# Optimization experiments

Measured on AMD Instinct MI355X. Metric: run time of the kernel, lower is better.

## Reference

```python
import jax, jax.numpy as jnp
import numpy as np

N_ITER = 4
NEG = -1e9


def _build_distmask(n):
    # dists='' -> 2 groups: upper triangular (j>i) and lower triangular (j<i); diag excluded
    iu = jnp.triu(jnp.ones((n, n), jnp.float32), 1)
    return jnp.stack([iu, iu.T], axis=0)  # (2, n, n)


def setup_inputs() -> dict:
    key = jax.random.key(0)
    k1, k2, k3 = jax.random.split(key, 3)
    B, N, D, H, G = 16, 256, 128, 8, 64
    x = jax.random.normal(k1, (B, N, D), jnp.float32)
    mask = jnp.ones((B, N), jnp.int32)
    ternary = jax.random.normal(k2, (2, D, D, H), jnp.float32)
    global_ = jax.random.normal(k3, (G, D, H), jnp.float32) / np.sqrt(D).astype(np.float32)
    return {"x": x, "mask": mask, "ternary": ternary, "global_": global_}


def reference(x, mask, ternary, global_):
    # x: (B,N,D) unary scores; mask: (B,N); ternary: (2,D,D,H); global_: (G,D,H)
    B, N, D = x.shape
    dm = _build_distmask(N)                       # (2,N,N)
    m1 = mask != 0                                # (B,N) valid tokens
    m2 = m1[:, :, None] & m1[:, None, :]          # (B,N,N) valid pairs
    pair_bias = jnp.where(m2[:, None, :, :], 0.0, NEG)  # (B,1,N,N); global cols stay unmasked

    Q_Z = x
    for _ in range(N_ITER):
        qz = jax.nn.softmax(Q_Z, axis=-1)         # (B,N,D) q(Z_i)
        # left[k,b,i,c,h] = sum_a qz[b,i,a] * ternary[k,a,c,h]
        left = jnp.einsum('bia,kach->kbich', qz, ternary)
        # H-node scores over local candidates: F[b,h,i,j] = sum_k dm[k,i,j] * sum_c left[k,b,i,c,h] qz[b,j,c]
        Fk = jnp.einsum('kbich,bjc->kbhij', left, qz)
        F = jnp.einsum('kbhij,kij->bhij', Fk, dm) + pair_bias
        # H-node scores over global candidates: G[b,h,i,g] = sum_a qz[b,i,a] global_[g,a,h]
        Gs = jnp.einsum('bia,gah->bhig', qz, global_)
        S = jnp.concatenate([F, Gs], axis=-1)     # (B,H,N,N+G), all-attn: joint softmax
        qh = jax.nn.softmax(S, axis=-1)           # async update: fresh q(H) used for Z update
        qh_loc, qh_glb = qh[..., :N], qh[..., N:]
        qhd = qh_loc[None] * dm[:, None, None]    # (2,B,H,N,N) distance-gated q(H)
        # right[k,b,j,a,h] = sum_c ternary[k,a,c,h] qz[b,j,c]  (message payload toward Z_i)
        right = jnp.einsum('kach,bjc->kbjah', ternary, qz)
        M1 = jnp.einsum('kbhij,kbjah->bia', qhd, right)   # message to dependent Z_i
        M2 = jnp.einsum('kbhij,kbich->bjc', qhd, left)    # message to head Z_j (block_msg=False)
        MG = jnp.einsum('bhig,gah->bia', qh_glb, global_)  # message from global nodes
        Q_Z = x + M1 + M2 + MG                    # regularize_Z=1, stepsize=1, damping=0
    return Q_Z                                    # output_prob=False -> unnormalized scores
```

## Files before the change

kernel.cpp:

```cpp
#include <hip/hip_runtime.h>
#include <hip/hip_bf16.h>

using bf16 = __hip_bfloat16;
typedef __bf16 bf16x8 __attribute__((ext_vector_type(8)));
typedef float f32x4 __attribute__((ext_vector_type(4)));
typedef unsigned short u16x8 __attribute__((ext_vector_type(8)));
typedef unsigned short u16x4 __attribute__((ext_vector_type(4)));

constexpr int B_ = 16, H_ = 8;
constexpr int BN = 4096;
constexpr int SW = 320;
constexpr float FNEG = -1000000000.0f;
constexpr size_t KOFF = (size_t)8 * 16 * 128 * 256;

__device__ __forceinline__ float b2f(bf16 v){ return __bfloat162float(v); }
__device__ __forceinline__ bf16 f2b(float v){ return __float2bfloat16(v); }
__device__ __forceinline__ bf16x8 ldf(const bf16* p){ return *(const bf16x8*)p; }
__device__ __forceinline__ f32x4 mfma16(bf16x8 a, bf16x8 b, f32x4 c){
  return __builtin_amdgcn_mfma_f32_16x16x32_bf16(a, b, c, 0, 0, 0);
}

__global__ __launch_bounds__(256) void k_prep(const float* __restrict__ tern,
                                              const float* __restrict__ glb,
                                              bf16* __restrict__ TL, bf16* __restrict__ TR,
                                              bf16* __restrict__ GB, bf16* __restrict__ GT){
  int t = blockIdx.x*256 + threadIdx.x;
  {
    int kh = t>>14, rest = t&16383;
    int k = kh>>3, h = kh&7;
    int r = rest>>7, cc = rest&127;
    TL[t] = f2b(tern[(((size_t)k*128 + cc)*128 + r)*8 + h]);
    TR[t] = f2b(tern[(((size_t)k*128 + r)*128 + cc)*8 + h]);
  }
  if (t < 65536){
    int h = t>>13, rest = t&8191;
    { int g = rest>>7, a = rest&127;
      GB[t] = f2b(glb[((size_t)g*128 + a)*8 + h]); }
    { int a = rest>>6, g = rest&63;
      GT[t] = f2b(glb[((size_t)g*128 + a)*8 + h]); }
  }
}

__global__ __launch_bounds__(256) void k_softmax_qz(const float* __restrict__ Q,
                                                    bf16* __restrict__ qzb){
  int row = blockIdx.x*4 + (threadIdx.x>>6);
  int lane = threadIdx.x&63;
  const float* q = Q + (size_t)row*128;
  float v0 = q[lane], v1 = q[lane+64];
  float m = fmaxf(v0, v1);
  #pragma unroll
  for (int o=32;o;o>>=1) m = fmaxf(m, __shfl_xor(m, o));
  float e0 = __expf(v0-m), e1 = __expf(v1-m), s = e0+e1;
  #pragma unroll
  for (int o=32;o;o>>=1) s += __shfl_xor(s, o);
  float inv = 1.f/s;
  bf16* o_ = qzb + (size_t)row*128;
  o_[lane] = f2b(e0*inv); o_[lane+64] = f2b(e1*inv);
}

__global__ __launch_bounds__(256) void k_proj(const bf16* __restrict__ qzb,
                                              const bf16* __restrict__ TL,
                                              const bf16* __restrict__ TR,
                                              bf16* __restrict__ left,
                                              bf16* __restrict__ LT2,
                                              bf16* __restrict__ RT2){
  const int z = blockIdx.z; const int kh = z & 15; const bool rightP = z >= 16;
  const int wi = threadIdx.x>>7, wj = (threadIdx.x>>6)&1;
  const int lane = threadIdx.x&63, lr = lane&15, kg = lane>>4;
  const int rb0 = blockIdx.x*64, cb = blockIdx.y*64;
  const int r0 = rb0 + wi*32, c0 = cb + wj*32;
  const bf16* A  = qzb + (size_t)r0*128;
  const bf16* Bb = (rightP ? TR : TL) + ((size_t)kh*128 + c0)*128;
  f32x4 acc[2][2] = {};
  #pragma unroll
  for (int k0=0;k0<128;k0+=32){
    bf16x8 a0 = ldf(A  + (size_t)lr*128      + k0 + kg*8);
    bf16x8 a1 = ldf(A  + (size_t)(lr+16)*128 + k0 + kg*8);
    bf16x8 b0 = ldf(Bb + (size_t)lr*128      + k0 + kg*8);
    bf16x8 b1 = ldf(Bb + (size_t)(lr+16)*128 + k0 + kg*8);
    acc[0][0]=mfma16(a0,b0,acc[0][0]); acc[0][1]=mfma16(a0,b1,acc[0][1]);
    acc[1][0]=mfma16(a1,b0,acc[1][0]); acc[1][1]=mfma16(a1,b1,acc[1][1]);
  }
  __shared__ unsigned short tl[64][68];
  #pragma unroll
  for (int fi=0;fi<2;fi++)
    #pragma unroll
    for (int fj=0;fj<2;fj++){
      u16x4 pk;
      #pragma unroll
      for (int r=0;r<4;r++) pk[r] = __builtin_bit_cast(unsigned short, f2b(acc[fi][fj][r]));
      *(u16x4*)&tl[wj*32 + fj*16 + lr][wi*32 + fi*16 + kg*4] = pk;
    }
  if (!rightP){
    #pragma unroll
    for (int fi=0;fi<2;fi++){
      int rb = r0 + fi*16 + kg*4;
      #pragma unroll
      for (int fj=0;fj<2;fj++){
        int col = c0 + fj*16 + lr;
        #pragma unroll
        for (int r=0;r<4;r++)
          left[((size_t)kh*BN + rb + r)*128 + col] = f2b(acc[fi][fj][r]);
      }
    }
  }
  __syncthreads();
  const int b = rb0 >> 8, jloc = rb0 & 255;
  const int col = threadIdx.x >> 2, seg = threadIdx.x & 3;
  bf16* O = rightP ? RT2 : LT2;
  unsigned short* dst = (unsigned short*)O +
      (((size_t)kh*16 + b)*128 + cb + col)*256 + jloc + seg*16;
  const unsigned short* src = &tl[col][seg*16];
  #pragma unroll
  for (int e=0;e<4;e++) *(u16x4*)(dst + e*4) = *(const u16x4*)(src + e*4);
}

__global__ __launch_bounds__(256) void k_FSM(const bf16* __restrict__ qzb,
                                             const bf16* __restrict__ left,
                                             const bf16* __restrict__ GB,
                                             const int* __restrict__ mask,
                                             bf16* __restrict__ qh,
                                             bf16* __restrict__ qhT2){
  const int bh = blockIdx.y, b = bh>>3, h = bh&7;
  const int ib4 = blockIdx.x;
  const int w = threadIdx.x>>6, lane = threadIdx.x&63;
  const int lr = lane&15, kg = lane>>4;
  const int i0 = ib4*64, iw = i0 + w*16;
  const int fd = iw>>4;
  const bf16* qzB = qzb + (size_t)b*256*128;
  const bf16* L0 = left + ((size_t)h*BN     + b*256 + iw)*128;
  const bf16* L1 = left + ((size_t)(8+h)*BN + b*256 + iw)*128;
  const bf16* GBh = GB + (size_t)h*64*128;
  f32x4 acc[20] = {}; f32x4 accD = {};
  #pragma unroll
  for (int k0=0;k0<128;k0+=32){
    bf16x8 aQ  = ldf(qzB + (size_t)(iw+lr)*128 + k0 + kg*8);
    bf16x8 aL0 = ldf(L0 + (size_t)lr*128 + k0 + kg*8);
    bf16x8 aL1 = ldf(L1 + (size_t)lr*128 + k0 + kg*8);
    #pragma unroll
    for (int f=0;f<16;f++){
      bf16x8 bf_ = ldf(qzB + (size_t)(f*16+lr)*128 + k0 + kg*8);
      acc[f] = mfma16((f>=fd)? aL0 : aL1, bf_, acc[f]);
      if (f==fd) accD = mfma16(aL1, bf_, accD);
    }
    #pragma unroll
    for (int f2=0;f2<4;f2++){
      bf16x8 bg = ldf(GBh + (size_t)(f2*16+lr)*128 + k0 + kg*8);
      acc[16+f2] = mfma16(aQ, bg, acc[16+f2]);
    }
  }
  const int* mb = mask + b*256;
  int mi[4];
  #pragma unroll
  for (int r=0;r<4;r++) mi[r] = mb[iw + kg*4 + r];
  float m[4] = {-3e38f,-3e38f,-3e38f,-3e38f};
  #pragma unroll
  for (int f=0;f<20;f++){
    if (f<16){
      int mj = mb[f*16 + lr];
      #pragma unroll
      for (int r=0;r<4;r++){
        float v = acc[f][r];
        if (f==fd){
          int d = lr - (kg*4+r);
          v = d>0 ? acc[f][r] : (d<0 ? accD[r] : 0.f);
        }
        v += (mi[r] && mj) ? 0.f : FNEG;
        acc[f][r] = v;
        m[r] = fmaxf(m[r], v);
      }
    } else {
      #pragma unroll
      for (int r=0;r<4;r++) m[r] = fmaxf(m[r], acc[f][r]);
    }
  }
  #pragma unroll
  for (int o=1;o<16;o<<=1)
    #pragma unroll
    for (int r=0;r<4;r++) m[r] = fmaxf(m[r], __shfl_xor(m[r], o));
  float s[4] = {0.f,0.f,0.f,0.f};
  #pragma unroll
  for (int f=0;f<20;f++)
    #pragma unroll
    for (int r=0;r<4;r++){ float e = __expf(acc[f][r]-m[r]); acc[f][r]=e; s[r]+=e; }
  #pragma unroll
  for (int o=1;o<16;o<<=1)
    #pragma unroll
    for (int r=0;r<4;r++) s[r] += __shfl_xor(s[r], o);
  float inv[4];
  #pragma unroll
  for (int r=0;r<4;r++) inv[r] = 1.f/s[r];
  __shared__ unsigned short t2[320][72];
  const int rowb = w*16 + kg*4;
  #pragma unroll
  for (int f=0;f<20;f++){
    u16x4 pk;
    #pragma unroll
    for (int r=0;r<4;r++) pk[r] = __builtin_bit_cast(unsigned short, f2b(acc[f][r]*inv[r]));
    *(u16x4*)&t2[f*16+lr][rowb] = pk;
  }
  __syncthreads();
  {
    const int j = threadIdx.x;
    unsigned short* dst = (unsigned short*)qhT2 + (((size_t)bh*4 + ib4)*256 + j)*64;
    #pragma unroll
    for (int e0=0;e0<64;e0+=8) *(u16x8*)(dst+e0) = *(const u16x8*)&t2[j][e0];
  }
  {
    const int row = threadIdx.x&63, seg = threadIdx.x>>6;
    unsigned short* dst = (unsigned short*)qh + ((size_t)bh*256 + i0 + row)*SW + seg*80;
    #pragma unroll
    for (int cc=0;cc<10;cc++){
      u16x8 pk;
      #pragma unroll
      for (int e=0;e<8;e++) pk[e] = t2[seg*80 + cc*8 + e][row];
      *(u16x8*)(dst + cc*8) = pk;
    }
  }
}

__global__ __launch_bounds__(256) void k_M2x(const bf16* __restrict__ qh,
                                             const bf16* __restrict__ qhT2,
                                             const bf16* __restrict__ RT2,
                                             const bf16* __restrict__ LT2,
                                             const bf16* __restrict__ GT,
                                             float* __restrict__ Mp){
  const int z = blockIdx.z;
  const int mode = z>>6, zz = z&63, b = zz>>2, hg = zz&3;
  const int wi = threadIdx.x>>7, wj = (threadIdx.x>>6)&1;
  const int lane = threadIdx.x&63, lr = lane&15, kg = lane>>4;
  const int r0 = blockIdx.x*64 + wi*32;
  const int c0 = blockIdx.y*64 + wj*32;
  f32x4 acc[2][2] = {};
  #pragma unroll
  for (int hh=0;hh<2;hh++){
    const int h = hg*2 + hh;
    const bf16* Bg = (mode ? LT2+KOFF : RT2) + ((size_t)h*16 + b)*128*256;
    const bf16* Bl = (mode ? LT2 : RT2+KOFF) + ((size_t)h*16 + b)*128*256;
    const bf16* A0 = mode ? qhT2 + (size_t)(b*8+h)*65536
                          : qh   + (size_t)(b*8+h)*256*SW;
    #pragma unroll
    for (int kt=0;kt<8;kt++){
      const int k0 = kt*32;
      const bool needG = (k0 >= r0), needL = (k0 <= r0+32);
      bf16x8 bg0{}, bg1{}, bl0{}, bl1{};
      if (needG){
        bg0 = ldf(Bg + (size_t)(c0+lr)*256    + k0 + kg*8);
        bg1 = ldf(Bg + (size_t)(c0+16+lr)*256 + k0 + kg*8);
      }
      if (needL){
        bl0 = ldf(Bl + (size_t)(c0+lr)*256    + k0 + kg*8);
        bl1 = ldf(Bl + (size_t)(c0+16+lr)*256 + k0 + kg*8);
      }
      #pragma unroll
      for (int fi=0;fi<2;fi++){
        const int ib = r0 + fi*16;
        bf16x8 a = (mode==0)
          ? ldf(A0 + (size_t)(ib+lr)*SW + k0 + kg*8)
          : ldf(A0 + (((size_t)(k0>>6))*256 + ib + lr)*64 + (k0&63) + kg*8);
        if (k0 >= ib + 16){
          acc[fi][0]=mfma16(a,bg0,acc[fi][0]); acc[fi][1]=mfma16(a,bg1,acc[fi][1]);
        } else if (k0 + 32 <= ib){
          acc[fi][0]=mfma16(a,bl0,acc[fi][0]); acc[fi][1]=mfma16(a,bl1,acc[fi][1]);
        } else {
          u16x8 u = __builtin_bit_cast(u16x8, a), ug, ul;
          const int tt = k0 + kg*8 - ib - lr;
          #pragma unroll
          for (int e=0;e<8;e++){
            ug[e] = (tt+e>0) ? u[e] : (unsigned short)0;
            ul[e] = (tt+e<0) ? u[e] : (unsigned short)0;
          }
          bf16x8 ag = __builtin_bit_cast(bf16x8, ug), al = __builtin_bit_cast(bf16x8, ul);
          acc[fi][0]=mfma16(ag,bg0,acc[fi][0]); acc[fi][1]=mfma16(ag,bg1,acc[fi][1]);
          acc[fi][0]=mfma16(al,bl0,acc[fi][0]); acc[fi][1]=mfma16(al,bl1,acc[fi][1]);
        }
      }
    }
    if (mode==0){
      const bf16* Bgl = GT + (size_t)h*128*64;
      #pragma unroll
      for (int kt=0;kt<2;kt++){
        const int k0 = kt*32;
        bf16x8 b0 = ldf(Bgl + (size_t)(c0+lr)*64    + k0 + kg*8);
        bf16x8 b1 = ldf(Bgl + (size_t)(c0+16+lr)*64 + k0 + kg*8);
        #pragma unroll
        for (int fi=0;fi<2;fi++){
          bf16x8 a = ldf(A0 + (size_t)(r0+fi*16+lr)*SW + 256 + k0 + kg*8);
          acc[fi][0]=mfma16(a,b0,acc[fi][0]); acc[fi][1]=mfma16(a,b1,acc[fi][1]);
        }
      }
    }
  }
  const int plane = mode*4 + hg;
  #pragma unroll
  for (int fi=0;fi<2;fi++)
    #pragma unroll
    for (int fj=0;fj<2;fj++)
      #pragma unroll
      for (int r=0;r<4;r++){
        int row = r0 + fi*16 + kg*4 + r;
        int col = c0 + fj*16 + lr;
        Mp[((size_t)plane*BN + b*256 + row)*128 + col] = acc[fi][fj][r];
      }
}

__global__ __launch_bounds__(256) void k_redqz(const float* __restrict__ x,
                                               const float* __restrict__ Mp,
                                               float* __restrict__ out,
                                               bf16* __restrict__ qzb){
  const int row = blockIdx.x*4 + (threadIdx.x>>6);
  const int lane = threadIdx.x&63;
  const size_t base = (size_t)row*128;
  float v0 = x[base + lane], v1 = x[base + 64 + lane];
  #pragma unroll
  for (int g=0;g<8;g++){
    v0 += Mp[(size_t)g*524288 + base + lane];
    v1 += Mp[(size_t)g*524288 + base + 64 + lane];
  }
  out[base + lane] = v0; out[base + 64 + lane] = v1;
  float m = fmaxf(v0, v1);
  #pragma unroll
  for (int o=32;o;o>>=1) m = fmaxf(m, __shfl_xor(m, o));
  float e0 = __expf(v0-m), e1 = __expf(v1-m), s = e0+e1;
  #pragma unroll
  for (int o=32;o;o>>=1) s += __shfl_xor(s, o);
  float inv = 1.f/s;
  qzb[base + lane] = f2b(e0*inv); qzb[base + 64 + lane] = f2b(e1*inv);
}

extern "C" void kernel_launch(void* const* d_in, const int* in_sizes, int n_in,
                              void* d_out, int out_size, void* d_ws, size_t ws_size,
                              hipStream_t stream) {
  (void)in_sizes; (void)n_in; (void)out_size; (void)ws_size;
  const float* x    = (const float*)d_in[0];
  const int*   mask = (const int*)d_in[1];
  const float* tern = (const float*)d_in[2];
  const float* glb  = (const float*)d_in[3];
  float* out = (float*)d_out;

  char* w = (char*)d_ws;
  auto alloc = [&](size_t bytes){ void* p = (void*)w; w += (bytes + 255) & ~(size_t)255; return p; };
  bf16* qzb   = (bf16*) alloc((size_t)BN*128*2);
  bf16* left  = (bf16*) alloc((size_t)16*BN*128*2);
  bf16* LT2   = (bf16*) alloc((size_t)16*16*128*256*2);
  bf16* RT2   = (bf16*) alloc((size_t)16*16*128*256*2);
  bf16* qh    = (bf16*) alloc((size_t)128*256*SW*2);
  bf16* qhT2  = (bf16*) alloc((size_t)128*4*256*64*2);
  float* Mp   = (float*)alloc((size_t)8*BN*128*4);
  bf16* TL    = (bf16*) alloc((size_t)16*128*128*2);
  bf16* TR    = (bf16*) alloc((size_t)16*128*128*2);
  bf16* GB    = (bf16*) alloc((size_t)8*64*128*2);
  bf16* GT    = (bf16*) alloc((size_t)8*64*128*2);

  k_prep<<<1024, 256, 0, stream>>>(tern, glb, TL, TR, GB, GT);
  k_softmax_qz<<<1024, 256, 0, stream>>>(x, qzb);

  for (int it = 0; it < 4; ++it){
    k_proj<<<dim3(64,2,32), 256, 0, stream>>>(qzb, TL, TR, left, LT2, RT2);
    k_FSM<<<dim3(4,128), 256, 0, stream>>>(qzb, left, GB, mask, qh, qhT2);
    k_M2x<<<dim3(4,2,128), 256, 0, stream>>>(qh, qhT2, RT2, LT2, GT, Mp);
    k_redqz<<<1024, 256, 0, stream>>>(x, Mp, out, qzb);
  }
}
```

Before: 551.0 us.

## Swizzle block indices, stage qz in LDS, split M2x per head

Result: no change. 545.9 us (-0.9%).

```diff
diff --git a/kernel.cpp b/kernel.cpp
--- a/kernel.cpp
+++ b/kernel.cpp
@@ -64,10 +64,13 @@
                                               bf16* __restrict__ left,
                                               bf16* __restrict__ LT2,
                                               bf16* __restrict__ RT2){
-  const int z = blockIdx.z; const int kh = z & 15; const bool rightP = z >= 16;
+  const int id = blockIdx.x;
+  const int swz = (id & 7)*512 + (id >> 3);
+  const int bx = swz & 63, by = (swz >> 6) & 1, z = swz >> 7;
+  const int kh = z & 15; const bool rightP = z >= 16;
   const int wi = threadIdx.x>>7, wj = (threadIdx.x>>6)&1;
   const int lane = threadIdx.x&63, lr = lane&15, kg = lane>>4;
-  const int rb0 = blockIdx.x*64, cb = blockIdx.y*64;
+  const int rb0 = bx*64, cb = by*64;
   const int r0 = rb0 + wi*32, c0 = cb + wj*32;
   const bf16* A  = qzb + (size_t)r0*128;
   const bf16* Bb = (rightP ? TR : TL) + ((size_t)kh*128 + c0)*128;
@@ -91,28 +94,29 @@
       for (int r=0;r<4;r++) pk[r] = __builtin_bit_cast(unsigned short, f2b(acc[fi][fj][r]));
       *(u16x4*)&tl[wj*32 + fj*16 + lr][wi*32 + fi*16 + kg*4] = pk;
     }
+  __syncthreads();
+  const int tt = threadIdx.x;
+  {
+    const int b = rb0 >> 8, jloc = rb0 & 255;
+    const int col = tt >> 2, seg = tt & 3;
+    bf16* O = rightP ? RT2 : LT2;
+    unsigned short* dst = (unsigned short*)O +
+        (((size_t)kh*16 + b)*128 + cb + col)*256 + jloc + seg*16;
+    const unsigned short* src = &tl[col][seg*16];
+    #pragma unroll
+    for (int e=0;e<4;e++) *(u16x4*)(dst + e*4) = *(const u16x4*)(src + e*4);
+  }
   if (!rightP){
-    #pragma unroll
-    for (int fi=0;fi<2;fi++){
-      int rb = r0 + fi*16 + kg*4;
-      #pragma unroll
-      for (int fj=0;fj<2;fj++){
-        int col = c0 + fj*16 + lr;
-        #pragma unroll
-        for (int r=0;r<4;r++)
-          left[((size_t)kh*BN + rb + r)*128 + col] = f2b(acc[fi][fj][r]);
-      }
-    }
-  }
-  __syncthreads();
-  const int b = rb0 >> 8, jloc = rb0 & 255;
-  const int col = threadIdx.x >> 2, seg = threadIdx.x & 3;
-  bf16* O = rightP ? RT2 : LT2;
-  unsigned short* dst = (unsigned short*)O +
-      (((size_t)kh*16 + b)*128 + cb + col)*256 + jloc + seg*16;
-  const unsigned short* src = &tl[col][seg*16];
-  #pragma unroll
-  for (int e=0;e<4;e++) *(u16x4*)(dst + e*4) = *(const u16x4*)(src + e*4);
+    const int row = tt & 63, cseg = tt >> 6;
+    u16x8 p0, p1;
+    #pragma unroll
+    for (int e=0;e<8;e++) p0[e] = tl[cseg*16+e][row];
+    #pragma unroll
+    for (int e=0;e<8;e++) p1[e] = tl[cseg*16+8+e][row];
+    unsigned short* dst = (unsigned short*)left +
+        ((size_t)kh*BN + rb0 + row)*128 + cb + cseg*16;
+    *(u16x8*)dst = p0; *(u16x8*)(dst+8) = p1;
+  }
 }
 
 __global__ __launch_bounds__(256) void k_FSM(const bf16* __restrict__ qzb,
@@ -121,8 +125,10 @@
                                              const int* __restrict__ mask,
                                              bf16* __restrict__ qh,
                                              bf16* __restrict__ qhT2){
-  const int bh = blockIdx.y, b = bh>>3, h = bh&7;
-  const int ib4 = blockIdx.x;
+  const int id = blockIdx.x;
+  const int swz = (id & 7)*64 + (id >> 3);
+  const int ib4 = swz & 3, bh = swz >> 2;
+  const int b = bh>>3, h = bh&7;
   const int w = threadIdx.x>>6, lane = threadIdx.x&63;
   const int lr = lane&15, kg = lane>>4;
   const int i0 = ib4*64, iw = i0 + w*16;
@@ -131,15 +137,36 @@
   const bf16* L0 = left + ((size_t)h*BN     + b*256 + iw)*128;
   const bf16* L1 = left + ((size_t)(8+h)*BN + b*256 + iw)*128;
   const bf16* GBh = GB + (size_t)h*64*128;
+
+  __shared__ unsigned short qt[2][8192];
+  __shared__ unsigned short t2[320][72];
+
+  const int tt = threadIdx.x;
+  const int sr = tt>>2, sk = (tt&3)*8;
+  u16x8 rg[4];
+  #pragma unroll
+  for (int c=0;c<4;c++)
+    rg[c] = *(const u16x8*)((const unsigned short*)qzB + (size_t)(c*64+sr)*128 + sk);
+  #pragma unroll
+  for (int c=0;c<4;c++)
+    *(u16x8*)&qt[0][(c*64+sr)*32 + sk] = rg[c];
+  __syncthreads();
+
   f32x4 acc[20] = {}; f32x4 accD = {};
   #pragma unroll
-  for (int k0=0;k0<128;k0+=32){
-    bf16x8 aQ  = ldf(qzB + (size_t)(iw+lr)*128 + k0 + kg*8);
+  for (int ks=0; ks<4; ks++){
+    const int k0 = ks*32; const int cur = ks&1;
+    if (ks<3){
+      #pragma unroll
+      for (int c=0;c<4;c++)
+        rg[c] = *(const u16x8*)((const unsigned short*)qzB + (size_t)(c*64+sr)*128 + k0+32 + sk);
+    }
+    bf16x8 aQ  = *(const bf16x8*)&qt[cur][(iw+lr)*32 + kg*8];
     bf16x8 aL0 = ldf(L0 + (size_t)lr*128 + k0 + kg*8);
     bf16x8 aL1 = ldf(L1 + (size_t)lr*128 + k0 + kg*8);
     #pragma unroll
     for (int f=0;f<16;f++){
-      bf16x8 bf_ = ldf(qzB + (size_t)(f*16+lr)*128 + k0 + kg*8);
+      bf16x8 bf_ = *(const bf16x8*)&qt[cur][(f*16+lr)*32 + kg*8];
       acc[f] = mfma16((f>=fd)? aL0 : aL1, bf_, acc[f]);
       if (f==fd) accD = mfma16(aL1, bf_, accD);
     }
@@ -148,6 +175,12 @@
       bf16x8 bg = ldf(GBh + (size_t)(f2*16+lr)*128 + k0 + kg*8);
       acc[16+f2] = mfma16(aQ, bg, acc[16+f2]);
     }
+    if (ks<3){
+      #pragma unroll
+      for (int c=0;c<4;c++)
+        *(u16x8*)&qt[cur^1][(c*64+sr)*32 + sk] = rg[c];
+    }
+    __syncthreads();
   }
   const int* mb = mask + b*256;
   int mi[4];
@@ -190,7 +223,6 @@
   float inv[4];
   #pragma unroll
   for (int r=0;r<4;r++) inv[r] = 1.f/s[r];
-  __shared__ unsigned short t2[320][72];
   const int rowb = w*16 + kg*4;
   #pragma unroll
   for (int f=0;f<20;f++){
@@ -201,13 +233,13 @@
   }
   __syncthreads();
   {
-    const int j = threadIdx.x;
+    const int j = tt;
     unsigned short* dst = (unsigned short*)qhT2 + (((size_t)bh*4 + ib4)*256 + j)*64;
     #pragma unroll
     for (int e0=0;e0<64;e0+=8) *(u16x8*)(dst+e0) = *(const u16x8*)&t2[j][e0];
   }
   {
-    const int row = threadIdx.x&63, seg = threadIdx.x>>6;
+    const int row = tt&63, seg = tt>>6;
     unsigned short* dst = (unsigned short*)qh + ((size_t)bh*256 + i0 + row)*SW + seg*80;
     #pragma unroll
     for (int cc=0;cc<10;cc++){
@@ -225,73 +257,72 @@
                                              const bf16* __restrict__ LT2,
                                              const bf16* __restrict__ GT,
                                              float* __restrict__ Mp){
-  const int z = blockIdx.z;
-  const int mode = z>>6, zz = z&63, b = zz>>2, hg = zz&3;
+  const int P = blockIdx.x;
+  const int cx = P & 7, t = P >> 3;
+  const int g = cx + ((t >> 3) << 3);
+  const int m = t & 7;
+  const int mode = g & 1, h = (g >> 1) & 7, b = g >> 4;
   const int wi = threadIdx.x>>7, wj = (threadIdx.x>>6)&1;
   const int lane = threadIdx.x&63, lr = lane&15, kg = lane>>4;
-  const int r0 = blockIdx.x*64 + wi*32;
-  const int c0 = blockIdx.y*64 + wj*32;
+  const int r0 = (m & 3)*64 + wi*32;
+  const int c0 = (m >> 2)*64 + wj*32;
+  const bf16* Bg = (mode ? LT2+KOFF : RT2) + ((size_t)h*16 + b)*128*256;
+  const bf16* Bl = (mode ? LT2 : RT2+KOFF) + ((size_t)h*16 + b)*128*256;
+  const bf16* A0 = mode ? qhT2 + (size_t)(b*8+h)*65536
+                        : qh   + (size_t)(b*8+h)*256*SW;
   f32x4 acc[2][2] = {};
   #pragma unroll
-  for (int hh=0;hh<2;hh++){
-    const int h = hg*2 + hh;
-    const bf16* Bg = (mode ? LT2+KOFF : RT2) + ((size_t)h*16 + b)*128*256;
-    const bf16* Bl = (mode ? LT2 : RT2+KOFF) + ((size_t)h*16 + b)*128*256;
-    const bf16* A0 = mode ? qhT2 + (size_t)(b*8+h)*65536
-                          : qh   + (size_t)(b*8+h)*256*SW;
-    #pragma unroll
-    for (int kt=0;kt<8;kt++){
+  for (int kt=0;kt<8;kt++){
+    const int k0 = kt*32;
+    const bool needG = (k0 >= r0), needL = (k0 <= r0+32);
+    bf16x8 bg0{}, bg1{}, bl0{}, bl1{};
+    if (needG){
+      bg0 = ldf(Bg + (size_t)(c0+lr)*256    + k0 + kg*8);
+      bg1 = ldf(Bg + (size_t)(c0+16+lr)*256 + k0 + kg*8);
+    }
+    if (needL){
+      bl0 = ldf(Bl + (size_t)(c0+lr)*256    + k0 + kg*8);
+      bl1 = ldf(Bl + (size_t)(c0+16+lr)*256 + k0 + kg*8);
+    }
+    #pragma unroll
+    for (int fi=0;fi<2;fi++){
+      const int ib = r0 + fi*16;
+      bf16x8 a = (mode==0)
+        ? ldf(A0 + (size_t)(ib+lr)*SW + k0 + kg*8)
+        : ldf(A0 + (((size_t)(k0>>6))*256 + ib + lr)*64 + (k0&63) + kg*8);
+      if (k0 >= ib + 16){
+        acc[fi][0]=mfma16(a,bg0,acc[fi][0]); acc[fi][1]=mfma16(a,bg1,acc[fi][1]);
+      } else if (k0 + 32 <= ib){
+        acc[fi][0]=mfma16(a,bl0,acc[fi][0]); acc[fi][1]=mfma16(a,bl1,acc[fi][1]);
+      } else {
+        u16x8 u = __builtin_bit_cast(u16x8, a), ug, ul;
+        const int d0 = k0 + kg*8 - ib - lr;
+        #pragma unroll
+        for (int e=0;e<8;e++){
+          ug[e] = (d0+e>0) ? u[e] : (unsigned short)0;
+          ul[e] = (d0+e<0) ? u[e] : (unsigned short)0;
+        }
+        bf16x8 ag = __builtin_bit_cast(bf16x8, ug), al = __builtin_bit_cast(bf16x8, ul);
+        acc[fi][0]=mfma16(ag,bg0,acc[fi][0]); acc[fi][1]=mfma16(ag,bg1,acc[fi][1]);
+        acc[fi][0]=mfma16(al,bl0,acc[fi][0]); acc[fi][1]=mfma16(al,bl1,acc[fi][1]);
+      }
+    }
+  }
+  if (mode==0){
+    const bf16* Bgl = GT + (size_t)h*128*64;
+    #pragma unroll
+    for (int kt=0;kt<2;kt++){
       const int k0 = kt*32;
-      const bool needG = (k0 >= r0), needL = (k0 <= r0+32);
-      bf16x8 bg0{}, bg1{}, bl0{}, bl1{};
-      if (needG){
-        bg0 = ldf(Bg + (size_t)(c0+lr)*256    + k0 + kg*8);
-        bg1 = ldf(Bg + (size_t)(c0+16+lr)*256 + k0 + kg*8);
+      bf16x8 b0 = ldf(Bgl + (size_t)(c0+lr)*64    + k0 + kg*8);
+      bf16x8 b1 = ldf(Bgl + (size_t)(c0+16+lr)*64 + k0 + kg*8);
+      #pragma unroll
+      for (int fi=0;fi<2;fi++){
+        bf16x8 a = ldf(A0 + (size_t)(r0+fi*16+lr)*SW + 256 + k0 + kg*8);
+        acc[fi][0]=mfma16(a,b0,acc[fi][0]); acc[fi][1]=mfma16(a,b1,acc[fi][1]);
       }
-      if (needL){
-        bl0 = ldf(Bl + (size_t)(c0+lr)*256    + k0 + kg*8);
-        bl1 = ldf(Bl + (size_t)(c0+16+lr)*256 + k0 + kg*8);
-      }
-      #pragma unroll
-      for (int fi=0;fi<2;fi++){
-        const int ib = r0 + fi*16;
-        bf16x8 a = (mode==0)
-          ? ldf(A0 + (size_t)(ib+lr)*SW + k0 + kg*8)
-          : ldf(A0 + (((size_t)(k0>>6))*256 + ib + lr)*64 + (k0&63) + kg*8);
-        if (k0 >= ib + 16){
-          acc[fi][0]=mfma16(a,bg0,acc[fi][0]); acc[fi][1]=mfma16(a,bg1,acc[fi][1]);
-        } else if (k0 + 32 <= ib){
-          acc[fi][0]=mfma16(a,bl0,acc[fi][0]); acc[fi][1]=mfma16(a,bl1,acc[fi][1]);
-        } else {
-          u16x8 u = __builtin_bit_cast(u16x8, a), ug, ul;
-          const int tt = k0 + kg*8 - ib - lr;
-          #pragma unroll
-          for (int e=0;e<8;e++){
-            ug[e] = (tt+e>0) ? u[e] : (unsigned short)0;
-            ul[e] = (tt+e<0) ? u[e] : (unsigned short)0;
-          }
-          bf16x8 ag = __builtin_bit_cast(bf16x8, ug), al = __builtin_bit_cast(bf16x8, ul);
-          acc[fi][0]=mfma16(ag,bg0,acc[fi][0]); acc[fi][1]=mfma16(ag,bg1,acc[fi][1]);
-          acc[fi][0]=mfma16(al,bl0,acc[fi][0]); acc[fi][1]=mfma16(al,bl1,acc[fi][1]);
-        }
-      }
-    }
-    if (mode==0){
-      const bf16* Bgl = GT + (size_t)h*128*64;
-      #pragma unroll
-      for (int kt=0;kt<2;kt++){
-        const int k0 = kt*32;
-        bf16x8 b0 = ldf(Bgl + (size_t)(c0+lr)*64    + k0 + kg*8);
-        bf16x8 b1 = ldf(Bgl + (size_t)(c0+16+lr)*64 + k0 + kg*8);
-        #pragma unroll
-        for (int fi=0;fi<2;fi++){
-          bf16x8 a = ldf(A0 + (size_t)(r0+fi*16+lr)*SW + 256 + k0 + kg*8);
-          acc[fi][0]=mfma16(a,b0,acc[fi][0]); acc[fi][1]=mfma16(a,b1,acc[fi][1]);
-        }
-      }
-    }
-  }
-  const int plane = mode*4 + hg;
+    }
+  }
+  const int plane = mode*8 + h;
   #pragma unroll
   for (int fi=0;fi<2;fi++)
     #pragma unroll
@@ -313,7 +344,7 @@
   const size_t base = (size_t)row*128;
   float v0 = x[base + lane], v1 = x[base + 64 + lane];
   #pragma unroll
-  for (int g=0;g<8;g++){
+  for (int g=0;g<16;g++){
     v0 += Mp[(size_t)g*524288 + base + lane];
     v1 += Mp[(size_t)g*524288 + base + 64 + lane];
   }
@@ -346,7 +377,7 @@
   bf16* RT2   = (bf16*) alloc((size_t)16*16*128*256*2);
   bf16* qh    = (bf16*) alloc((size_t)128*256*SW*2);
   bf16* qhT2  = (bf16*) alloc((size_t)128*4*256*64*2);
-  float* Mp   = (float*)alloc((size_t)8*BN*128*4);
+  float* Mp   = (float*)alloc((size_t)16*BN*128*4);
   bf16* TL    = (bf16*) alloc((size_t)16*128*128*2);
   bf16* TR    = (bf16*) alloc((size_t)16*128*128*2);
   bf16* GB    = (bf16*) alloc((size_t)8*64*128*2);
@@ -356,9 +387,9 @@
   k_softmax_qz<<<1024, 256, 0, stream>>>(x, qzb);
 
   for (int it = 0; it < 4; ++it){
-    k_proj<<<dim3(64,2,32), 256, 0, stream>>>(qzb, TL, TR, left, LT2, RT2);
-    k_FSM<<<dim3(4,128), 256, 0, stream>>>(qzb, left, GB, mask, qh, qhT2);
-    k_M2x<<<dim3(4,2,128), 256, 0, stream>>>(qh, qhT2, RT2, LT2, GT, Mp);
+    k_proj<<<4096, 256, 0, stream>>>(qzb, TL, TR, left, LT2, RT2);
+    k_FSM<<<512, 256, 0, stream>>>(qzb, left, GB, mask, qh, qhT2);
+    k_M2x<<<2048, 256, 0, stream>>>(qh, qhT2, RT2, LT2, GT, Mp);
     k_redqz<<<1024, 256, 0, stream>>>(x, Mp, out, qzb);
   }
 }
```
